# Optimization experiments

Measured on AMD Instinct MI355X. Metric: run time of the kernel, lower is better.

The kernel has to match this reference:

```python
import jax, jax.numpy as jnp
import numpy as np

IN_CAPS, IN_DIM, OUT_CAPS, OUT_DIM = 2048, 8, 32, 16
NUM_ROUTING = 3
EPS = 1e-9


def squash(s):
    # s: [..., out_dim]
    s2 = jnp.sum(s * s, axis=-1, keepdims=True)
    return (s2 / (1.0 + s2)) * (s / jnp.sqrt(s2 + EPS))


def setup_inputs() -> dict:
    key = jax.random.key(0)
    kx, kw = jax.random.split(key)
    x = jax.random.normal(kx, (64, IN_CAPS, IN_DIM), dtype=jnp.float32)
    W = jax.random.normal(kw, (1, IN_CAPS, OUT_CAPS, OUT_DIM, IN_DIM), dtype=jnp.float32) * 0.01
    return {"x": x, "W": W}


def reference(x, W):
    # u_hat[b,i,o,j] = sum_d W[0,i,o,j,d] * x[b,i,d]
    u_hat = jnp.einsum('iojd,bid->bioj', W[0], x)  # [B, in_caps, out_caps, out_dim]
    b_ij = jnp.zeros(u_hat.shape[:3], dtype=u_hat.dtype)  # [B, in_caps, out_caps]
    v_j = None
    for r in range(NUM_ROUTING):
        c_ij = jax.nn.softmax(b_ij, axis=2)[..., None]  # [B, in, out, 1]
        s_j = jnp.sum(c_ij * u_hat, axis=1)             # [B, out, out_dim]
        v_j = squash(s_j)
        if r < NUM_ROUTING - 1:
            b_ij = b_ij + jnp.einsum('bioj,boj->bio', u_hat, v_j)
    return v_j
```

## Files before the change

kernel.cpp:

```cpp
#include <hip/hip_runtime.h>
#include <math.h>


#define IC 2048
#define ID 8
#define OC 32
#define OD 16
#define B_N 64
#define S_ELEMS (B_N * OC * OD)
#define IB 16
#define ISTR (IC / IB)
#define BPB 16
#define BG (B_N / BPB)

__device__ __forceinline__ void gll16(const float4* g, float4* l)
{
    __builtin_amdgcn_global_load_lds(
        (const __attribute__((address_space(1))) void*)g,
        (__attribute__((address_space(3))) void*)l,
        16, 0, 0);
}

template <int CTRL>
__device__ __forceinline__ float dpp_add(float x)
{
    union { float f; int i; } a, b;
    a.f = x;
    b.i = __builtin_amdgcn_update_dpp(0, a.i, CTRL, 0xF, 0xF, true);
    return x + b.f;
}


template <int FIRST>
__launch_bounds__(256, 2)
__global__ void caps_pass(const float* __restrict__ Wg,
                          const float* __restrict__ xg,
                          const float* __restrict__ vs,
                          float* __restrict__ part)
{
    __shared__ float4 Wl[2][1024];
    __shared__ float4 xsh[2][BPB * 2];

    const int tid  = threadIdx.x;
    const int lane = tid & 63;
    const int w    = tid >> 6;
    const int o    = lane & 31;
    const int jh   = lane >> 5;

    const int is   = blockIdx.x & (ISTR - 1);
    const int bg   = blockIdx.x >> 7;
    const int bblk = bg * BPB;

    const float4* wq = (const float4*)Wg;

    float4 va[4], vb[4];
    if (!FIRST) {
#pragma unroll
        for (int n = 0; n < 4; ++n) {
            const float* vp =
                vs + (size_t)(bblk + w * 4 + n) * (OC * OD) + o * OD + jh * 8;
            va[n] = ((const float4*)vp)[0];
            vb[n] = ((const float4*)vp)[1];
        }
    }

    float acc[4][8];
#pragma unroll
    for (int n = 0; n < 4; ++n)
#pragma unroll
        for (int jj = 0; jj < 8; ++jj) acc[n][jj] = 0.0f;

    {
        const int ig = is * IB;
        const size_t wb0 = (size_t)ig * 1024;
#pragma unroll
        for (int s = 0; s < 4; ++s) {
            const int D = s * 256 + tid;
            const int orow = D >> 5;
            const int f = orow * 32 + ((D & 31) ^ orow);
            gll16(wq + wb0 + f, &Wl[0][D]);
        }
        if (tid < 32)
            xsh[0][tid] = ((const float4*)xg)
                [((size_t)(bblk + (tid >> 1)) * IC + ig) * 2 + (tid & 1)];
    }

    for (int il = 0; il < IB; ++il) {
        const int p = il & 1;
        __syncthreads();

        float4 gx = {};
        const bool more = (il + 1 < IB);
        if (more) {
            const int ig = is * IB + il + 1;
            const size_t wb0 = (size_t)ig * 1024;
#pragma unroll
            for (int s = 0; s < 4; ++s) {
                const int D = s * 256 + tid;
                const int orow = D >> 5;
                const int f = orow * 32 + ((D & 31) ^ orow);
                gll16(wq + wb0 + f, &Wl[p ^ 1][D]);
            }
            if (tid < 32)
                gx = ((const float4*)xg)
                    [((size_t)(bblk + (tid >> 1)) * IC + ig) * 2 + (tid & 1)];
        }

        float4 wA[8], wB[8];
        const int row = o * 32;
#pragma unroll
        for (int jj = 0; jj < 8; ++jj) {
            const int ca = (jh * 16 + jj * 2) ^ o;
            wA[jj] = Wl[p][row + ca];
            wB[jj] = Wl[p][row + (ca ^ 1)];
        }

#pragma unroll
        for (int n = 0; n < 4; ++n) {
            const float4 xa = xsh[p][(w * 4 + n) * 2];
            const float4 xb = xsh[p][(w * 4 + n) * 2 + 1];
            float u[8];
#pragma unroll
            for (int jj = 0; jj < 8; ++jj) {
                float t = wA[jj].x * xa.x;
                t = fmaf(wA[jj].y, xa.y, t);
                t = fmaf(wA[jj].z, xa.z, t);
                t = fmaf(wA[jj].w, xa.w, t);
                t = fmaf(wB[jj].x, xb.x, t);
                t = fmaf(wB[jj].y, xb.y, t);
                t = fmaf(wB[jj].z, xb.z, t);
                t = fmaf(wB[jj].w, xb.w, t);
                u[jj] = t;
            }
            float cc;
            if (FIRST) {
                cc = 1.0f;
            } else {
                float bp = u[0] * va[n].x;
                bp = fmaf(u[1], va[n].y, bp);
                bp = fmaf(u[2], va[n].z, bp);
                bp = fmaf(u[3], va[n].w, bp);
                bp = fmaf(u[4], vb[n].x, bp);
                bp = fmaf(u[5], vb[n].y, bp);
                bp = fmaf(u[6], vb[n].z, bp);
                bp = fmaf(u[7], vb[n].w, bp);
                bp += __shfl_xor(bp, 32);
                const float e = __expf(bp);
                float t = dpp_add<0xB1>(e);
                t = dpp_add<0x4E>(t);
                t = dpp_add<0x124>(t);
                t = dpp_add<0x128>(t);
                const float se = t + __shfl_xor(t, 16);
                cc = e * __builtin_amdgcn_rcpf(se);
            }
#pragma unroll
            for (int jj = 0; jj < 8; ++jj)
                acc[n][jj] = fmaf(cc, u[jj], acc[n][jj]);
        }

        if (more && tid < 32) xsh[p ^ 1][tid] = gx;
    }

    const float scale = FIRST ? (1.0f / 32.0f) : 1.0f;
#pragma unroll
    for (int n = 0; n < 4; ++n) {
        float* dst = part + (size_t)is * S_ELEMS
                   + (size_t)(bblk + w * 4 + n) * (OC * OD) + o * OD + jh * 8;
        float4 lo = {acc[n][0] * scale, acc[n][1] * scale,
                     acc[n][2] * scale, acc[n][3] * scale};
        float4 hi = {acc[n][4] * scale, acc[n][5] * scale,
                     acc[n][6] * scale, acc[n][7] * scale};
        ((float4*)dst)[0] = lo;
        ((float4*)dst)[1] = hi;
    }
}

template <int MODE>
__launch_bounds__(256, 4)
__global__ void caps_reduce(const float* __restrict__ part,
                            float* __restrict__ vsum,
                            float* __restrict__ out)
{
    __shared__ float red[4][64];
    const int tid  = threadIdx.x;
    const int w    = tid >> 6;
    const int lane = tid & 63;
    const int e0   = blockIdx.x * 64;

    float s = 0.0f;
#pragma unroll 8
    for (int k = w; k < ISTR; k += 4)
        s += part[(size_t)k * S_ELEMS + e0 + lane];
    red[w][lane] = s;
    __syncthreads();

    if (tid < 64) {
        const float t = red[0][tid] + red[1][tid] + red[2][tid] + red[3][tid];
        float s2 = t * t;
        s2 += __shfl_xor(s2, 1);
        s2 += __shfl_xor(s2, 2);
        s2 += __shfl_xor(s2, 4);
        s2 += __shfl_xor(s2, 8);
        const float v = t * (s2 / ((1.0f + s2) * sqrtf(s2 + 1e-9f)));
        const int e = e0 + tid;
        if (MODE == 0)      vsum[e] = v;
        else if (MODE == 1) vsum[e] += v;
        else                out[e] = v;
    }
}

extern "C" void kernel_launch(void* const* d_in, const int* in_sizes, int n_in,
                              void* d_out, int out_size, void* d_ws, size_t ws_size,
                              hipStream_t stream)
{
    const float* x = (const float*)d_in[0];
    const float* W = (const float*)d_in[1];
    float* out = (float*)d_out;

    float* part = (float*)d_ws;
    float* vsum = part + (size_t)ISTR * S_ELEMS;

    const dim3 gP(BG * ISTR);
    const dim3 bP(256);
    const dim3 gR(S_ELEMS / 64);
    const dim3 bR(256);

    caps_pass<1><<<gP, bP, 0, stream>>>(W, x, nullptr, part);
    caps_reduce<0><<<gR, bR, 0, stream>>>(part, vsum, out);
    caps_pass<0><<<gP, bP, 0, stream>>>(W, x, vsum, part);
    caps_reduce<1><<<gR, bR, 0, stream>>>(part, vsum, out);
    caps_pass<0><<<gP, bP, 0, stream>>>(W, x, vsum, part);
    caps_reduce<2><<<gR, bR, 0, stream>>>(part, vsum, out);
}
```

Measured before the change: 169.8 us.

## Halve per-block input-capsule chunk and restructure W register loads for occupancy

```diff
diff --git a/kernel.cpp b/kernel.cpp
--- a/kernel.cpp
+++ b/kernel.cpp
@@ -8,7 +8,7 @@
 #define OD 16
 #define B_N 64
 #define S_ELEMS (B_N * OC * OD)
-#define IB 16
+#define IB 8
 #define ISTR (IC / IB)
 #define BPB 16
 #define BG (B_N / BPB)
@@ -32,7 +32,7 @@
 
 
 template <int FIRST>
-__launch_bounds__(256, 2)
+__launch_bounds__(256, 3)
 __global__ void caps_pass(const float* __restrict__ Wg,
                           const float* __restrict__ xg,
                           const float* __restrict__ vs,
@@ -48,7 +48,7 @@
     const int jh   = lane >> 5;
 
     const int is   = blockIdx.x & (ISTR - 1);
-    const int bg   = blockIdx.x >> 7;
+    const int bg   = blockIdx.x >> 8;
     const int bblk = bg * BPB;
 
     const float4* wq = (const float4*)Wg;
@@ -106,44 +106,51 @@
                     [((size_t)(bblk + (tid >> 1)) * IC + ig) * 2 + (tid & 1)];
         }
 
-        float4 wA[8], wB[8];
+        float u[4][8];
         const int row = o * 32;
 #pragma unroll
-        for (int jj = 0; jj < 8; ++jj) {
-            const int ca = (jh * 16 + jj * 2) ^ o;
-            wA[jj] = Wl[p][row + ca];
-            wB[jj] = Wl[p][row + (ca ^ 1)];
+        for (int half = 0; half < 2; ++half) {
+            float4 wA[4], wB[4];
+#pragma unroll
+            for (int q = 0; q < 4; ++q) {
+                const int jj = half * 4 + q;
+                const int ca = (jh * 16 + jj * 2) ^ o;
+                wA[q] = Wl[p][row + ca];
+                wB[q] = Wl[p][row + (ca ^ 1)];
+            }
+#pragma unroll
+            for (int n = 0; n < 4; ++n) {
+                const float4 xa = xsh[p][(w * 4 + n) * 2];
+                const float4 xb = xsh[p][(w * 4 + n) * 2 + 1];
+#pragma unroll
+                for (int q = 0; q < 4; ++q) {
+                    float t = wA[q].x * xa.x;
+                    t = fmaf(wA[q].y, xa.y, t);
+                    t = fmaf(wA[q].z, xa.z, t);
+                    t = fmaf(wA[q].w, xa.w, t);
+                    t = fmaf(wB[q].x, xb.x, t);
+                    t = fmaf(wB[q].y, xb.y, t);
+                    t = fmaf(wB[q].z, xb.z, t);
+                    t = fmaf(wB[q].w, xb.w, t);
+                    u[n][half * 4 + q] = t;
+                }
+            }
         }
 
 #pragma unroll
         for (int n = 0; n < 4; ++n) {
-            const float4 xa = xsh[p][(w * 4 + n) * 2];
-            const float4 xb = xsh[p][(w * 4 + n) * 2 + 1];
-            float u[8];
-#pragma unroll
-            for (int jj = 0; jj < 8; ++jj) {
-                float t = wA[jj].x * xa.x;
-                t = fmaf(wA[jj].y, xa.y, t);
-                t = fmaf(wA[jj].z, xa.z, t);
-                t = fmaf(wA[jj].w, xa.w, t);
-                t = fmaf(wB[jj].x, xb.x, t);
-                t = fmaf(wB[jj].y, xb.y, t);
-                t = fmaf(wB[jj].z, xb.z, t);
-                t = fmaf(wB[jj].w, xb.w, t);
-                u[jj] = t;
-            }
             float cc;
             if (FIRST) {
                 cc = 1.0f;
             } else {
-                float bp = u[0] * va[n].x;
-                bp = fmaf(u[1], va[n].y, bp);
-                bp = fmaf(u[2], va[n].z, bp);
-                bp = fmaf(u[3], va[n].w, bp);
-                bp = fmaf(u[4], vb[n].x, bp);
-                bp = fmaf(u[5], vb[n].y, bp);
-                bp = fmaf(u[6], vb[n].z, bp);
-                bp = fmaf(u[7], vb[n].w, bp);
+                float bp = u[n][0] * va[n].x;
+                bp = fmaf(u[n][1], va[n].y, bp);
+                bp = fmaf(u[n][2], va[n].z, bp);
+                bp = fmaf(u[n][3], va[n].w, bp);
+                bp = fmaf(u[n][4], vb[n].x, bp);
+                bp = fmaf(u[n][5], vb[n].y, bp);
+                bp = fmaf(u[n][6], vb[n].z, bp);
+                bp = fmaf(u[n][7], vb[n].w, bp);
                 bp += __shfl_xor(bp, 32);
                 const float e = __expf(bp);
                 float t = dpp_add<0xB1>(e);
@@ -155,7 +162,7 @@
             }
 #pragma unroll
             for (int jj = 0; jj < 8; ++jj)
-                acc[n][jj] = fmaf(cc, u[jj], acc[n][jj]);
+                acc[n][jj] = fmaf(cc, u[n][jj], acc[n][jj]);
         }
 
         if (more && tid < 32) xsh[p ^ 1][tid] = gx;
```

Measured after the change: 407.6 us. 140% more time.

## Deepen W prefetch to a 4-buffer pipeline and preload x via LDS DMA

Applied to the files above, without the earlier changes.

```diff
diff --git a/kernel.cpp b/kernel.cpp
--- a/kernel.cpp
+++ b/kernel.cpp
@@ -38,8 +38,8 @@
                           const float* __restrict__ vs,
                           float* __restrict__ part)
 {
-    __shared__ float4 Wl[2][1024];
-    __shared__ float4 xsh[2][BPB * 2];
+    __shared__ float4 Wl[4][1024];
+    __shared__ float4 xs[BPB * 32];
 
     const int tid  = threadIdx.x;
     const int lane = tid & 63;
@@ -50,8 +50,10 @@
     const int is   = blockIdx.x & (ISTR - 1);
     const int bg   = blockIdx.x >> 7;
     const int bblk = bg * BPB;
+    const int ig0  = is * IB;
 
     const float4* wq = (const float4*)Wg;
+    const float4* xq = (const float4*)xg;
 
     float4 va[4], vb[4];
     if (!FIRST) {
@@ -70,55 +72,45 @@
 #pragma unroll
         for (int jj = 0; jj < 8; ++jj) acc[n][jj] = 0.0f;
 
-    {
-        const int ig = is * IB;
-        const size_t wb0 = (size_t)ig * 1024;
+    auto stage = [&](int t) {
+        const size_t wb0 = (size_t)(ig0 + t) * 1024;
+        float4* dst = Wl[t & 3];
 #pragma unroll
         for (int s = 0; s < 4; ++s) {
             const int D = s * 256 + tid;
             const int orow = D >> 5;
             const int f = orow * 32 + ((D & 31) ^ orow);
-            gll16(wq + wb0 + f, &Wl[0][D]);
-        }
-        if (tid < 32)
-            xsh[0][tid] = ((const float4*)xg)
-                [((size_t)(bblk + (tid >> 1)) * IC + ig) * 2 + (tid & 1)];
-    }
-
-    for (int il = 0; il < IB; ++il) {
-        const int p = il & 1;
-        __syncthreads();
-
-        float4 gx = {};
-        const bool more = (il + 1 < IB);
-        if (more) {
-            const int ig = is * IB + il + 1;
-            const size_t wb0 = (size_t)ig * 1024;
-#pragma unroll
-            for (int s = 0; s < 4; ++s) {
-                const int D = s * 256 + tid;
-                const int orow = D >> 5;
-                const int f = orow * 32 + ((D & 31) ^ orow);
-                gll16(wq + wb0 + f, &Wl[p ^ 1][D]);
-            }
-            if (tid < 32)
-                gx = ((const float4*)xg)
-                    [((size_t)(bblk + (tid >> 1)) * IC + ig) * 2 + (tid & 1)];
-        }
-
+            gll16(wq + wb0 + f, dst + D);
+        }
+    };
+
+    stage(0);
+    stage(1);
+    {
+#pragma unroll
+        for (int q = 0; q < 2; ++q) {
+            const int s = q * 256 + tid;
+            const int b = s >> 5;
+            const int r = s & 31;
+            gll16(xq + ((size_t)(bblk + b) * IC + ig0) * 2 + r, &xs[s]);
+        }
+    }
+
+    auto compute = [&](int il) {
         float4 wA[8], wB[8];
+        const float4* buf = Wl[il & 3];
         const int row = o * 32;
 #pragma unroll
         for (int jj = 0; jj < 8; ++jj) {
             const int ca = (jh * 16 + jj * 2) ^ o;
-            wA[jj] = Wl[p][row + ca];
-            wB[jj] = Wl[p][row + (ca ^ 1)];
+            wA[jj] = buf[row + ca];
+            wB[jj] = buf[row + (ca ^ 1)];
         }
 
 #pragma unroll
         for (int n = 0; n < 4; ++n) {
-            const float4 xa = xsh[p][(w * 4 + n) * 2];
-            const float4 xb = xsh[p][(w * 4 + n) * 2 + 1];
+            const float4 xa = xs[(w * 4 + n) * 32 + il * 2];
+            const float4 xb = xs[(w * 4 + n) * 32 + il * 2 + 1];
             float u[8];
 #pragma unroll
             for (int jj = 0; jj < 8; ++jj) {
@@ -157,9 +149,20 @@
             for (int jj = 0; jj < 8; ++jj)
                 acc[n][jj] = fmaf(cc, u[jj], acc[n][jj]);
         }
-
-        if (more && tid < 32) xsh[p ^ 1][tid] = gx;
-    }
+    };
+
+    for (int il = 0; il < IB - 2; ++il) {
+        stage(il + 2);
+        asm volatile("s_waitcnt vmcnt(8)" ::: "memory");
+        __builtin_amdgcn_s_barrier();
+        compute(il);
+    }
+    asm volatile("s_waitcnt vmcnt(4)" ::: "memory");
+    __builtin_amdgcn_s_barrier();
+    compute(IB - 2);
+    asm volatile("s_waitcnt vmcnt(0)" ::: "memory");
+    __builtin_amdgcn_s_barrier();
+    compute(IB - 1);
 
     const float scale = FIRST ? (1.0f / 32.0f) : 1.0f;
 #pragma unroll
```

Result: no change. 170.2 us (+0.2%).

## Store partial sums in fp16, halve input-capsule chunk, preload all x tiles

Applied to the files above, without the earlier changes.

```diff
diff --git a/kernel.cpp b/kernel.cpp
--- a/kernel.cpp
+++ b/kernel.cpp
@@ -1,4 +1,5 @@
 #include <hip/hip_runtime.h>
+#include <hip/hip_fp16.h>
 #include <math.h>
 
 
@@ -8,7 +9,7 @@
 #define OD 16
 #define B_N 64
 #define S_ELEMS (B_N * OC * OD)
-#define IB 16
+#define IB 8
 #define ISTR (IC / IB)
 #define BPB 16
 #define BG (B_N / BPB)
@@ -36,10 +37,10 @@
 __global__ void caps_pass(const float* __restrict__ Wg,
                           const float* __restrict__ xg,
                           const float* __restrict__ vs,
-                          float* __restrict__ part)
+                          __half* __restrict__ part)
 {
     __shared__ float4 Wl[2][1024];
-    __shared__ float4 xsh[2][BPB * 2];
+    __shared__ float4 xs[BPB * 2 * IB];
 
     const int tid  = threadIdx.x;
     const int lane = tid & 63;
@@ -48,10 +49,12 @@
     const int jh   = lane >> 5;
 
     const int is   = blockIdx.x & (ISTR - 1);
-    const int bg   = blockIdx.x >> 7;
+    const int bg   = blockIdx.x >> 8;
     const int bblk = bg * BPB;
+    const int ig0  = is * IB;
 
     const float4* wq = (const float4*)Wg;
+    const float4* xq = (const float4*)xg;
 
     float4 va[4], vb[4];
     if (!FIRST) {
@@ -70,41 +73,30 @@
 #pragma unroll
         for (int jj = 0; jj < 8; ++jj) acc[n][jj] = 0.0f;
 
-    {
-        const int ig = is * IB;
-        const size_t wb0 = (size_t)ig * 1024;
-#pragma unroll
-        for (int s = 0; s < 4; ++s) {
-            const int D = s * 256 + tid;
+    auto stage = [&](int t, int parity) {
+        const size_t wb0 = (size_t)(ig0 + t) * 1024;
+        float4* dst = Wl[parity];
+#pragma unroll
+        for (int s4 = 0; s4 < 4; ++s4) {
+            const int D = s4 * 256 + tid;
             const int orow = D >> 5;
             const int f = orow * 32 + ((D & 31) ^ orow);
-            gll16(wq + wb0 + f, &Wl[0][D]);
-        }
-        if (tid < 32)
-            xsh[0][tid] = ((const float4*)xg)
-                [((size_t)(bblk + (tid >> 1)) * IC + ig) * 2 + (tid & 1)];
+            gll16(wq + wb0 + f, dst + D);
+        }
+    };
+
+    stage(0, 0);
+    {
+        const int b  = tid >> 4;
+        const int rr = tid & 15;
+        gll16(xq + ((size_t)(bblk + b) * IC + ig0) * 2 + rr, &xs[tid]);
     }
 
     for (int il = 0; il < IB; ++il) {
         const int p = il & 1;
         __syncthreads();
 
-        float4 gx = {};
-        const bool more = (il + 1 < IB);
-        if (more) {
-            const int ig = is * IB + il + 1;
-            const size_t wb0 = (size_t)ig * 1024;
-#pragma unroll
-            for (int s = 0; s < 4; ++s) {
-                const int D = s * 256 + tid;
-                const int orow = D >> 5;
-                const int f = orow * 32 + ((D & 31) ^ orow);
-                gll16(wq + wb0 + f, &Wl[p ^ 1][D]);
-            }
-            if (tid < 32)
-                gx = ((const float4*)xg)
-                    [((size_t)(bblk + (tid >> 1)) * IC + ig) * 2 + (tid & 1)];
-        }
+        if (il + 1 < IB) stage(il + 1, p ^ 1);
 
         float4 wA[8], wB[8];
         const int row = o * 32;
@@ -117,8 +109,8 @@
 
 #pragma unroll
         for (int n = 0; n < 4; ++n) {
-            const float4 xa = xsh[p][(w * 4 + n) * 2];
-            const float4 xb = xsh[p][(w * 4 + n) * 2 + 1];
+            const float4 xa = xs[(w * 4 + n) * 16 + il * 2];
+            const float4 xb = xs[(w * 4 + n) * 16 + il * 2 + 1];
             float u[8];
 #pragma unroll
             for (int jj = 0; jj < 8; ++jj) {
@@ -157,27 +149,24 @@
             for (int jj = 0; jj < 8; ++jj)
                 acc[n][jj] = fmaf(cc, u[jj], acc[n][jj]);
         }
-
-        if (more && tid < 32) xsh[p ^ 1][tid] = gx;
     }
 
     const float scale = FIRST ? (1.0f / 32.0f) : 1.0f;
 #pragma unroll
     for (int n = 0; n < 4; ++n) {
-        float* dst = part + (size_t)is * S_ELEMS
-                   + (size_t)(bblk + w * 4 + n) * (OC * OD) + o * OD + jh * 8;
-        float4 lo = {acc[n][0] * scale, acc[n][1] * scale,
-                     acc[n][2] * scale, acc[n][3] * scale};
-        float4 hi = {acc[n][4] * scale, acc[n][5] * scale,
-                     acc[n][6] * scale, acc[n][7] * scale};
-        ((float4*)dst)[0] = lo;
-        ((float4*)dst)[1] = hi;
+        __half* dst = part + (size_t)is * S_ELEMS
+                    + (size_t)(bblk + w * 4 + n) * (OC * OD) + o * OD + jh * 8;
+        union { __half h[8]; uint4 u4; } pk;
+#pragma unroll
+        for (int jj = 0; jj < 8; ++jj)
+            pk.h[jj] = __float2half(acc[n][jj] * scale);
+        *(uint4*)dst = pk.u4;
     }
 }
 
 template <int MODE>
 __launch_bounds__(256, 4)
-__global__ void caps_reduce(const float* __restrict__ part,
+__global__ void caps_reduce(const __half* __restrict__ part,
                             float* __restrict__ vsum,
                             float* __restrict__ out)
 {
@@ -190,7 +179,7 @@
     float s = 0.0f;
 #pragma unroll 8
     for (int k = w; k < ISTR; k += 4)
-        s += part[(size_t)k * S_ELEMS + e0 + lane];
+        s += __half2float(part[(size_t)k * S_ELEMS + e0 + lane]);
     red[w][lane] = s;
     __syncthreads();
 
@@ -217,8 +206,8 @@
     const float* W = (const float*)d_in[1];
     float* out = (float*)d_out;
 
-    float* part = (float*)d_ws;
-    float* vsum = part + (size_t)ISTR * S_ELEMS;
+    __half* part = (__half*)d_ws;
+    float* vsum = (float*)((char*)d_ws + (size_t)ISTR * S_ELEMS * sizeof(__half));
 
     const dim3 gP(BG * ISTR);
     const dim3 bP(256);
```

Measured after the change: 167.1 us. No clear change (-1.6%).
